# Optimization experiments

Hardware: AMD Instinct MI355X
Metric: run time of the kernel (lower is better)

The kernel has to match this reference:

```python
import jax, jax.numpy as jnp
import numpy as np

SEG = 24      # segment_size
NH = 8        # n_heads
THETA = 10000.0


def setup_inputs() -> dict:
    key = jax.random.key(0)
    ks = jax.random.split(key, 6)
    B, T, H, W, D = 8, 96, 32, 32, 64
    in_dim = SEG * D          # 1536
    hid_dim = (SEG // 2) * D  # 768
    n_seg = T // SEG          # 4
    x = jax.random.normal(ks[0], (B, T, H, W, D), dtype=jnp.float32)
    # rotary frequencies: freqs_cis[t, j] = exp(i * t * theta^{-2j/hid_dim})
    inv = 1.0 / (THETA ** (np.arange(0, hid_dim, 2, dtype=np.float32) / hid_dim))
    ang = np.arange(n_seg, dtype=np.float32)[:, None] * inv[None, :]  # (n, hid/2)
    freqs_cos = jnp.asarray(np.cos(ang), dtype=jnp.float32)
    freqs_sin = jnp.asarray(np.sin(ang), dtype=jnp.float32)
    s = 0.02
    Wq = jax.random.normal(ks[1], (in_dim, hid_dim), dtype=jnp.float32) * s
    Wk = jax.random.normal(ks[2], (in_dim, hid_dim), dtype=jnp.float32) * s
    Wv = jax.random.normal(ks[3], (in_dim, hid_dim), dtype=jnp.float32) * s
    Wo = jax.random.normal(ks[4], (hid_dim, in_dim), dtype=jnp.float32) * s
    bo = jnp.zeros((in_dim,), dtype=jnp.float32)
    return {"x": x, "freqs_cos": freqs_cos, "freqs_sin": freqs_sin,
            "Wq": Wq, "Wk": Wk, "Wv": Wv, "Wo": Wo, "bo": bo}


def _rope(q, cos, sin):
    # q: (b, n, hid); pairs (even, odd) rotated by complex multiply
    q2 = q.reshape(*q.shape[:-1], -1, 2)
    qr = q2[..., 0] * cos - q2[..., 1] * sin
    qi = q2[..., 0] * sin + q2[..., 1] * cos
    return jnp.stack([qr, qi], axis=-1).reshape(q.shape)


def reference(x, freqs_cos, freqs_sin, Wq, Wk, Wv, Wo, bo):
    B, T, H, W, D = x.shape
    n = T // SEG
    hid = Wq.shape[1]
    hd = hid // NH
    # (b t h w d) -> ((b h w) n (p d)) ; T divisible by SEG so no padding
    xr = jnp.transpose(x, (0, 2, 3, 1, 4)).reshape(B * H * W, T, D)
    xs = xr.reshape(B * H * W, n, SEG * D)
    q = jnp.einsum('bne,eh->bnh', xs, Wq)
    k = jnp.einsum('bne,eh->bnh', xs, Wk)
    v = jnp.einsum('bne,eh->bnh', xs, Wv)
    cos, sin = freqs_cos[:n][None], freqs_sin[:n][None]  # (1, n, hid/2)
    q = _rope(q, cos, sin)
    k = _rope(k, cos, sin)
    # split heads: b n (h d) -> b h n d
    def heads(t):
        return jnp.transpose(t.reshape(B * H * W, n, NH, hd), (0, 2, 1, 3))
    qh, kh, vh = heads(q), heads(k), heads(v)
    scores = jnp.einsum('bhnd,bhmd->bhnm', qh, kh) / jnp.sqrt(jnp.float32(hd))
    attn = jax.nn.softmax(scores, axis=-1)
    o = jnp.einsum('bhnm,bhmd->bhnd', attn, vh)
    o = jnp.transpose(o, (0, 2, 1, 3)).reshape(B * H * W, n, hid)
    o = jnp.einsum('bnh,he->bne', o, Wo) + bo
    # b n (p d) -> b (n p) d -> (B,T,H,W,D)
    o = o.reshape(B * H * W, T, D)
    o = o.reshape(B, H, W, T, D)
    return jnp.transpose(o, (0, 3, 1, 2, 4))
```

## Files before the change

### kernel.cpp

```cpp
#include <hip/hip_runtime.h>
#include <hip/hip_bf16.h>

using bf16 = __hip_bfloat16;
using short8 = __attribute__((ext_vector_type(8))) short;
using floatx4 = __attribute__((ext_vector_type(4))) float;

#define NSEG 4
#define HID 768
#define INDIM 1536
#define NQKV 2304
#define NHEADS 8
#define HD 96

__device__ inline unsigned short f2b(float v) {
  union { float f; unsigned u; } c; c.f = v;
  unsigned r = c.u + 0x7FFF + ((c.u >> 16) & 1);
  return (unsigned short)(r >> 16);
}

__device__ inline void gload16(const void* g, void* l) {
  __builtin_amdgcn_global_load_lds(
      (const __attribute__((address_space(1))) unsigned int*)g,
      (__attribute__((address_space(3))) unsigned int*)l, 16, 0, 0);
}

__global__ __launch_bounds__(256) void transpose_w(
    const float* __restrict__ src, bf16* __restrict__ dst, int K, int C) {
  __shared__ unsigned short tile[32][33];
  const int c0 = blockIdx.x * 32, k0 = blockIdx.y * 32;
  const int tx = threadIdx.x, ty = threadIdx.y;
#pragma unroll
  for (int i = 0; i < 4; ++i)
    tile[ty + 8 * i][tx] = f2b(src[(size_t)(k0 + ty + 8 * i) * C + c0 + tx]);
  __syncthreads();
  unsigned short* d = (unsigned short*)dst;
#pragma unroll
  for (int i = 0; i < 4; ++i)
    d[(size_t)(c0 + ty + 8 * i) * K + k0 + tx] = tile[tx][ty + 8 * i];
}

__global__ __launch_bounds__(256) void convert_x(
    const float* __restrict__ x, bf16* __restrict__ xb) {
  const size_t i = ((size_t)blockIdx.x * 256 + threadIdx.x) * 8;
  float4 a = *(const float4*)(x + i);
  float4 b = *(const float4*)(x + i + 4);
  union { uint4 u; unsigned short s[8]; } r;
  r.s[0] = f2b(a.x); r.s[1] = f2b(a.y); r.s[2] = f2b(a.z); r.s[3] = f2b(a.w);
  r.s[4] = f2b(b.x); r.s[5] = f2b(b.y); r.s[6] = f2b(b.z); r.s[7] = f2b(b.w);
  *(uint4*)(xb + i) = r.u;
}

__global__ __launch_bounds__(256, 2) void gemm_qkv(
    const bf16* __restrict__ xb, const bf16* __restrict__ wT,
    bf16* __restrict__ qkv) {
  __shared__ __align__(16) short As[128 * 32];
  __shared__ __align__(16) short Bs[128 * 32];
  const int tid = threadIdx.x;
  const int n0 = blockIdx.x * 128;
  const int m0 = blockIdx.y * 128;
  const int lane = tid & 63, wave = tid >> 6;
  const int wm = (wave >> 1) * 64, wn = (wave & 1) * 64;
  const int l15 = lane & 15, quad = lane >> 4;
  const int srow = wave * 16 + (lane >> 2);
  const int sch = (lane & 3) * 8;
  floatx4 acc[4][4] = {};

  const int mA0 = m0 + srow, mA1 = m0 + 64 + srow;
  const int rA0 = mA0 >> 2, nA0 = mA0 & 3;
  const int rA1 = mA1 >> 2, nA1 = mA1 & 3;
  const size_t baseA0 =
      ((size_t)((rA0 >> 10) * 96 + nA0 * 24) * 1024 + (rA0 & 1023)) * 64;
  const size_t baseA1 =
      ((size_t)((rA1 >> 10) * 96 + nA1 * 24) * 1024 + (rA1 & 1023)) * 64;
  const bf16* bB0 = wT + (size_t)(n0 + srow) * INDIM + sch;
  const bf16* bB1 = wT + (size_t)(n0 + 64 + srow) * INDIM + sch;

  short* asb0 = &As[wave * 512];
  short* asb1 = &As[2048 + wave * 512];
  short* bsb0 = &Bs[wave * 512];
  short* bsb1 = &Bs[2048 + wave * 512];

  for (int kt = 0; kt < 48; ++kt) {
    const int k0 = kt * 32;
    const int p = kt >> 1;
    const int dlo = (kt & 1) * 32 + sch;
    __syncthreads();
    gload16(xb + baseA0 + (size_t)p * 65536 + dlo, asb0);
    gload16(xb + baseA1 + (size_t)p * 65536 + dlo, asb1);
    gload16(bB0 + k0, bsb0);
    gload16(bB1 + k0, bsb1);
    __syncthreads();
    short8 af[4], bg[4];
#pragma unroll
    for (int t = 0; t < 4; ++t) {
      af[t] = *(const short8*)&As[(wm + t * 16 + l15) * 32 + quad * 8];
      bg[t] = *(const short8*)&Bs[(wn + t * 16 + l15) * 32 + quad * 8];
    }
#pragma unroll
    for (int ti = 0; ti < 4; ++ti)
#pragma unroll
      for (int tj = 0; tj < 4; ++tj)
        acc[ti][tj] = __builtin_amdgcn_mfma_f32_16x16x32_bf16(
            af[ti], bg[tj], acc[ti][tj], 0, 0, 0);
  }
#pragma unroll
  for (int ti = 0; ti < 4; ++ti)
#pragma unroll
    for (int tj = 0; tj < 4; ++tj)
#pragma unroll
      for (int reg = 0; reg < 4; ++reg) {
        const int row = m0 + wm + ti * 16 + quad * 4 + reg;
        const int col = n0 + wn + tj * 16 + l15;
        qkv[(size_t)row * NQKV + col] = __float2bfloat16(acc[ti][tj][reg]);
      }
}

__global__ __launch_bounds__(256) void attn_kernel(
    const bf16* __restrict__ qkv, const float* __restrict__ fcos,
    const float* __restrict__ fsin, bf16* __restrict__ obuf) {
  constexpr int SF_LD = 2312;
  __shared__ float sf[NSEG][SF_LD];
  __shared__ float ssc[NHEADS][NSEG][NSEG];
  __shared__ float sat[NHEADS][NSEG][NSEG];
  const int r = blockIdx.x;
  const int tid = threadIdx.x;
  const bf16* base = qkv + (size_t)r * NSEG * NQKV;

  for (int cid = tid; cid < (NSEG * NQKV) / 8; cid += 256) {
    const int n = cid / (NQKV / 8);
    const int c = (cid % (NQKV / 8)) * 8;
    uint4 u = *(const uint4*)(base + (size_t)n * NQKV + c);
    const bf16* h = reinterpret_cast<const bf16*>(&u);
#pragma unroll
    for (int j = 0; j < 8; ++j) sf[n][c + j] = __bfloat162float(h[j]);
  }
  __syncthreads();

  for (int idx = tid; idx < NSEG * (HID / 2); idx += 256) {
    const int n = idx / (HID / 2), j = idx % (HID / 2);
    const float c = fcos[n * (HID / 2) + j];
    const float s = fsin[n * (HID / 2) + j];
    float q0 = sf[n][2 * j], q1 = sf[n][2 * j + 1];
    sf[n][2 * j] = q0 * c - q1 * s;
    sf[n][2 * j + 1] = q0 * s + q1 * c;
    float k0 = sf[n][HID + 2 * j], k1 = sf[n][HID + 2 * j + 1];
    sf[n][HID + 2 * j] = k0 * c - k1 * s;
    sf[n][HID + 2 * j + 1] = k0 * s + k1 * c;
  }
  __syncthreads();

  if (tid < 128) {
    const int h = tid >> 4, n = (tid >> 2) & 3, m = tid & 3;
    const float* qp = &sf[n][h * HD];
    const float* kp = &sf[m][HID + h * HD];
    float s = 0.f;
#pragma unroll 8
    for (int i = 0; i < HD; ++i) s += qp[i] * kp[i];
    ssc[h][n][m] = s * 0.10206207261596575f;
  }
  __syncthreads();

  if (tid < 32) {
    const int h = tid >> 2, n = tid & 3;
    float mx = ssc[h][n][0];
#pragma unroll
    for (int m = 1; m < 4; ++m) mx = fmaxf(mx, ssc[h][n][m]);
    float e[4], sum = 0.f;
#pragma unroll
    for (int m = 0; m < 4; ++m) { e[m] = __expf(ssc[h][n][m] - mx); sum += e[m]; }
    const float inv = 1.f / sum;
#pragma unroll
    for (int m = 0; m < 4; ++m) sat[h][n][m] = e[m] * inv;
  }
  __syncthreads();

  for (int idx = tid; idx < NSEG * HID; idx += 256) {
    const int n = idx / HID, c = idx % HID, h = c / HD;
    float s = 0.f;
#pragma unroll
    for (int m = 0; m < 4; ++m) s += sat[h][n][m] * sf[m][2 * HID + c];
    obuf[((size_t)r * NSEG + n) * HID + c] = __float2bfloat16(s);
  }
}

__global__ __launch_bounds__(256, 2) void gemm_out(
    const bf16* __restrict__ A, const bf16* __restrict__ wT,
    const float* __restrict__ bo, float* __restrict__ out) {
  __shared__ __align__(16) short As[128 * 32];
  __shared__ __align__(16) short Bs[128 * 32];
  const int tid = threadIdx.x;
  const int n0 = blockIdx.x * 128;
  const int m0 = blockIdx.y * 128;
  const int lane = tid & 63, wave = tid >> 6;
  const int wm = (wave >> 1) * 64, wn = (wave & 1) * 64;
  const int l15 = lane & 15, quad = lane >> 4;
  const int srow = wave * 16 + (lane >> 2);
  const int sch = (lane & 3) * 8;
  floatx4 acc[4][4] = {};

  const bf16* aB0 = A + (size_t)(m0 + srow) * HID + sch;
  const bf16* aB1 = A + (size_t)(m0 + 64 + srow) * HID + sch;
  const bf16* bB0 = wT + (size_t)(n0 + srow) * HID + sch;
  const bf16* bB1 = wT + (size_t)(n0 + 64 + srow) * HID + sch;

  short* asb0 = &As[wave * 512];
  short* asb1 = &As[2048 + wave * 512];
  short* bsb0 = &Bs[wave * 512];
  short* bsb1 = &Bs[2048 + wave * 512];

  for (int kt = 0; kt < 24; ++kt) {
    const int k0 = kt * 32;
    __syncthreads();
    gload16(aB0 + k0, asb0);
    gload16(aB1 + k0, asb1);
    gload16(bB0 + k0, bsb0);
    gload16(bB1 + k0, bsb1);
    __syncthreads();
    short8 af[4], bg[4];
#pragma unroll
    for (int t = 0; t < 4; ++t) {
      af[t] = *(const short8*)&As[(wm + t * 16 + l15) * 32 + quad * 8];
      bg[t] = *(const short8*)&Bs[(wn + t * 16 + l15) * 32 + quad * 8];
    }
#pragma unroll
    for (int ti = 0; ti < 4; ++ti)
#pragma unroll
      for (int tj = 0; tj < 4; ++tj)
        acc[ti][tj] = __builtin_amdgcn_mfma_f32_16x16x32_bf16(
            af[ti], bg[tj], acc[ti][tj], 0, 0, 0);
  }
#pragma unroll
  for (int ti = 0; ti < 4; ++ti)
#pragma unroll
    for (int tj = 0; tj < 4; ++tj)
#pragma unroll
      for (int reg = 0; reg < 4; ++reg) {
        const int row = m0 + wm + ti * 16 + quad * 4 + reg;
        const int col = n0 + wn + tj * 16 + l15;
        const float v = acc[ti][tj][reg] + bo[col];
        const int r = row >> 2, n = row & 3;
        const int b = r >> 10, hw = r & 1023;
        const int p = col >> 6, d = col & 63;
        const size_t dst =
            ((size_t)((b * 96 + n * 24 + p) * 1024 + hw)) * 64 + d;
        out[dst] = v;
      }
}

extern "C" void kernel_launch(void* const* d_in, const int* in_sizes, int n_in,
                              void* d_out, int out_size, void* d_ws,
                              size_t ws_size, hipStream_t stream) {
  const float* x = (const float*)d_in[0];
  const float* fcos = (const float*)d_in[1];
  const float* fsin = (const float*)d_in[2];
  const float* Wq = (const float*)d_in[3];
  const float* Wk = (const float*)d_in[4];
  const float* Wv = (const float*)d_in[5];
  const float* Wo = (const float*)d_in[6];
  const float* bo = (const float*)d_in[7];
  float* out = (float*)d_out;

  char* ws = (char*)d_ws;
  bf16* wqkvT = (bf16*)ws;
  bf16* woT = (bf16*)(ws + 7077888);
  bf16* qkv = (bf16*)(ws + 9437184);
  bf16* obuf = (bf16*)(ws + 160432128);
  bf16* xb = (bf16*)d_out;

  dim3 tb(32, 8);
  transpose_w<<<dim3(24, 48), tb, 0, stream>>>(Wq, wqkvT, INDIM, HID);
  transpose_w<<<dim3(24, 48), tb, 0, stream>>>(Wk, wqkvT + (size_t)HID * INDIM, INDIM, HID);
  transpose_w<<<dim3(24, 48), tb, 0, stream>>>(Wv, wqkvT + (size_t)2 * HID * INDIM, INDIM, HID);
  transpose_w<<<dim3(48, 24), tb, 0, stream>>>(Wo, woT, HID, INDIM);

  convert_x<<<24576, 256, 0, stream>>>(x, xb);
  gemm_qkv<<<dim3(18, 256), 256, 0, stream>>>(xb, wqkvT, qkv);
  attn_kernel<<<8192, 256, 0, stream>>>(qkv, fcos, fsin, obuf);
  gemm_out<<<dim3(12, 256), 256, 0, stream>>>(obuf, woT, bo, out);
}
```

Measured before the change: 827.2 us.

## Rewrite QKV and output GEMMs with 256x256 tiles, double-buffered swizzled LDS pipeline

Both GEMMs move from 128x128 tiles with two syncthreads per 32-wide K step to 256x256 tiles on 512 threads. They use a 64-wide K step and double-buffered LDS filled by direct global-to-LDS loads, interleaved with MFMA phases under explicit vmcnt waits and barriers. LDS addresses are XOR-swizzled to avoid bank conflicts, blocks are remapped for L2 locality, and s_setprio is raised around the MFMA bursts. This aims to hide memory latency and raise arithmetic intensity, at the cost of 128KB LDS per block, high register pressure, and delicate manual synchronisation.

```diff
diff --git a/kernel.cpp b/kernel.cpp
--- a/kernel.cpp
+++ b/kernel.cpp
@@ -23,6 +23,43 @@
       (const __attribute__((address_space(1))) unsigned int*)g,
       (__attribute__((address_space(3))) unsigned int*)l, 16, 0, 0);
 }
+
+#define MEMFENCE asm volatile("" ::: "memory")
+#define BARRIER do { MEMFENCE; __builtin_amdgcn_s_barrier(); MEMFENCE; } while (0)
+
+#define PHASE(par, q, LOADB, STAGES, VMW) do {                                 \
+    short8 a00 = *(const short8*)(lA + (par)*65536 + (q)*2048);                \
+    short8 a01 = *(const short8*)(lA + (par)*65536 + (q)*2048 + 16384);        \
+    short8 a10 = *(const short8*)(lA + (par)*65536 + (q)*2048 + 1024);         \
+    short8 a11 = *(const short8*)(lA + (par)*65536 + (q)*2048 + 1024 + 16384); \
+    if (LOADB) {                                                               \
+      _Pragma("unroll")                                                        \
+      for (int fn = 0; fn < 4; ++fn) {                                         \
+        bfr[fn][0] = *(const short8*)(lB + (par)*65536 + fn*1024);             \
+        bfr[fn][1] = *(const short8*)(lB + (par)*65536 + fn*1024 + 16384);     \
+      }                                                                        \
+    }                                                                          \
+    STAGES;                                                                    \
+    BARRIER;                                                                   \
+    __builtin_amdgcn_s_setprio(1);                                             \
+    _Pragma("unroll")                                                          \
+    for (int fn = 0; fn < 4; ++fn) {                                           \
+      acc[2*(q)][fn]   = __builtin_amdgcn_mfma_f32_16x16x32_bf16(              \
+          a00, bfr[fn][0], acc[2*(q)][fn], 0, 0, 0);                           \
+      acc[2*(q)][fn]   = __builtin_amdgcn_mfma_f32_16x16x32_bf16(              \
+          a01, bfr[fn][1], acc[2*(q)][fn], 0, 0, 0);                           \
+      acc[2*(q)+1][fn] = __builtin_amdgcn_mfma_f32_16x16x32_bf16(              \
+          a10, bfr[fn][0], acc[2*(q)+1][fn], 0, 0, 0);                         \
+      acc[2*(q)+1][fn] = __builtin_amdgcn_mfma_f32_16x16x32_bf16(              \
+          a11, bfr[fn][1], acc[2*(q)+1][fn], 0, 0, 0);                         \
+    }                                                                          \
+    __builtin_amdgcn_s_setprio(0);                                             \
+    VMW;                                                                       \
+    BARRIER;                                                                   \
+  } while (0)
+
+#define VM4 do { asm volatile("s_waitcnt vmcnt(4)" ::: "memory"); } while (0)
+#define VM0 do { asm volatile("s_waitcnt vmcnt(0)" ::: "memory"); } while (0)
 
 __global__ __launch_bounds__(256) void transpose_w(
     const float* __restrict__ src, bf16* __restrict__ dst, int K, int C) {
@@ -50,68 +87,84 @@
   *(uint4*)(xb + i) = r.u;
 }
 
-__global__ __launch_bounds__(256, 2) void gemm_qkv(
+__global__ __launch_bounds__(512, 2) void gemm_qkv(
     const bf16* __restrict__ xb, const bf16* __restrict__ wT,
     bf16* __restrict__ qkv) {
-  __shared__ __align__(16) short As[128 * 32];
-  __shared__ __align__(16) short Bs[128 * 32];
+  __shared__ __align__(16) char lds[131072];
   const int tid = threadIdx.x;
-  const int n0 = blockIdx.x * 128;
-  const int m0 = blockIdx.y * 128;
   const int lane = tid & 63, wave = tid >> 6;
-  const int wm = (wave >> 1) * 64, wn = (wave & 1) * 64;
+  const int wr = wave >> 2, wc = wave & 3;
   const int l15 = lane & 15, quad = lane >> 4;
+
+  const int lt = (blockIdx.x & 7) * 144 + (blockIdx.x >> 3);
+  const int n0 = (lt % 9) * 256;
+  const int m0 = (lt / 9) * 256;
+
   const int srow = wave * 16 + (lane >> 2);
-  const int sch = (lane & 3) * 8;
-  floatx4 acc[4][4] = {};
-
-  const int mA0 = m0 + srow, mA1 = m0 + 64 + srow;
-  const int rA0 = mA0 >> 2, nA0 = mA0 & 3;
-  const int rA1 = mA1 >> 2, nA1 = mA1 & 3;
-  const size_t baseA0 =
-      ((size_t)((rA0 >> 10) * 96 + nA0 * 24) * 1024 + (rA0 & 1023)) * 64;
-  const size_t baseA1 =
-      ((size_t)((rA1 >> 10) * 96 + nA1 * 24) * 1024 + (rA1 & 1023)) * 64;
-  const bf16* bB0 = wT + (size_t)(n0 + srow) * INDIM + sch;
-  const bf16* bB1 = wT + (size_t)(n0 + 64 + srow) * INDIM + sch;
-
-  short* asb0 = &As[wave * 512];
-  short* asb1 = &As[2048 + wave * 512];
-  short* bsb0 = &Bs[wave * 512];
-  short* bsb1 = &Bs[2048 + wave * 512];
-
-  for (int kt = 0; kt < 48; ++kt) {
-    const int k0 = kt * 32;
-    const int p = kt >> 1;
-    const int dlo = (kt & 1) * 32 + sch;
-    __syncthreads();
-    gload16(xb + baseA0 + (size_t)p * 65536 + dlo, asb0);
-    gload16(xb + baseA1 + (size_t)p * 65536 + dlo, asb1);
-    gload16(bB0 + k0, bsb0);
-    gload16(bB1 + k0, bsb1);
-    __syncthreads();
-    short8 af[4], bg[4];
-#pragma unroll
-    for (int t = 0; t < 4; ++t) {
-      af[t] = *(const short8*)&As[(wm + t * 16 + l15) * 32 + quad * 8];
-      bg[t] = *(const short8*)&Bs[(wn + t * 16 + l15) * 32 + quad * 8];
-    }
-#pragma unroll
-    for (int ti = 0; ti < 4; ++ti)
-#pragma unroll
-      for (int tj = 0; tj < 4; ++tj)
-        acc[ti][tj] = __builtin_amdgcn_mfma_f32_16x16x32_bf16(
-            af[ti], bg[tj], acc[ti][tj], 0, 0, 0);
-  }
-#pragma unroll
-  for (int ti = 0; ti < 4; ++ti)
-#pragma unroll
-    for (int tj = 0; tj < 4; ++tj)
+  const int dswz = ((lane & 3) * 8) ^ ((lane & 32) >> 1);
+  const bf16* asrc[2];
+  const bf16* bsrc[2];
+#pragma unroll
+  for (int h = 0; h < 2; ++h) {
+    const int m = m0 + h * 128 + srow;
+    const int r = m >> 2, n = m & 3;
+    const int b = r >> 10, hw = r & 1023;
+    asrc[h] = xb + ((size_t)((b * 96 + n * 24) * 1024 + hw)) * 64 + dswz;
+    bsrc[h] = wT + (size_t)(n0 + h * 128 + srow) * INDIM + dswz;
+  }
+  char* sdst = lds + wave * 1024;
+
+#define STAGE_QA(kt, h) do {                                   \
+    char* d_ = sdst + (((kt) & 1) * 65536) + (h) * 8192;       \
+    const bf16* s_ = asrc[h] + (size_t)(kt) * 65536;           \
+    gload16(s_, d_);                                           \
+    gload16(s_ + 32, d_ + 16384);                              \
+  } while (0)
+#define STAGE_QB(kt, h) do {                                   \
+    char* d_ = sdst + 32768 + (((kt) & 1) * 65536) + (h) * 8192; \
+    const bf16* s_ = bsrc[h] + (size_t)(kt) * 64;              \
+    gload16(s_, d_);                                           \
+    gload16(s_ + 32, d_ + 16384);                              \
+  } while (0)
+
+  const int lofs = l15 * 64 + ((quad * 16) ^ ((l15 & 8) << 2));
+  const char* lA = lds + wr * 8192 + lofs;
+  const char* lB = lds + 32768 + wc * 4096 + lofs;
+
+  floatx4 acc[8][4] = {};
+  short8 bfr[4][2];
+
+  STAGE_QB(0, 0); STAGE_QB(0, 1); STAGE_QA(0, 0); STAGE_QA(0, 1);
+  STAGE_QB(1, 0); STAGE_QB(1, 1);
+  VM4;
+  BARRIER;
+
+  const int NKT = 24;
+  for (int i = 0; i < 12; ++i) {
+    const int a = 2 * i;
+    PHASE(0, 0, 1, { STAGE_QA(a + 1, 0); }, {});
+    PHASE(0, 1, 0, { STAGE_QA(a + 1, 1); }, {});
+    PHASE(0, 2, 0, { if (a + 2 < NKT) STAGE_QB(a + 2, 0); }, {});
+    PHASE(0, 3, 0, { if (a + 2 < NKT) STAGE_QB(a + 2, 1); },
+          { if (a + 2 < NKT) VM4; else VM0; });
+    PHASE(1, 0, 1, { if (a + 2 < NKT) STAGE_QA(a + 2, 0); }, {});
+    PHASE(1, 1, 0, { if (a + 2 < NKT) STAGE_QA(a + 2, 1); }, {});
+    PHASE(1, 2, 0, { if (a + 3 < NKT) STAGE_QB(a + 3, 0); }, {});
+    PHASE(1, 3, 0, { if (a + 3 < NKT) STAGE_QB(a + 3, 1); },
+          { if (a + 3 < NKT) VM4; else VM0; });
+  }
+#undef STAGE_QA
+#undef STAGE_QB
+
+#pragma unroll
+  for (int fm = 0; fm < 8; ++fm)
+#pragma unroll
+    for (int fn = 0; fn < 4; ++fn)
 #pragma unroll
       for (int reg = 0; reg < 4; ++reg) {
-        const int row = m0 + wm + ti * 16 + quad * 4 + reg;
-        const int col = n0 + wn + tj * 16 + l15;
-        qkv[(size_t)row * NQKV + col] = __float2bfloat16(acc[ti][tj][reg]);
+        const int row = m0 + wr * 128 + fm * 16 + quad * 4 + reg;
+        const int col = n0 + wc * 64 + fn * 16 + l15;
+        qkv[(size_t)row * NQKV + col] = __float2bfloat16(acc[fm][fn][reg]);
       }
 }
 
@@ -183,61 +236,81 @@
   }
 }
 
-__global__ __launch_bounds__(256, 2) void gemm_out(
-    const bf16* __restrict__ A, const bf16* __restrict__ wT,
+__global__ __launch_bounds__(512, 2) void gemm_out(
+    const bf16* __restrict__ Ao, const bf16* __restrict__ wT,
     const float* __restrict__ bo, float* __restrict__ out) {
-  __shared__ __align__(16) short As[128 * 32];
-  __shared__ __align__(16) short Bs[128 * 32];
+  __shared__ __align__(16) char lds[131072];
   const int tid = threadIdx.x;
-  const int n0 = blockIdx.x * 128;
-  const int m0 = blockIdx.y * 128;
   const int lane = tid & 63, wave = tid >> 6;
-  const int wm = (wave >> 1) * 64, wn = (wave & 1) * 64;
+  const int wr = wave >> 2, wc = wave & 3;
   const int l15 = lane & 15, quad = lane >> 4;
+
+  const int lt = (blockIdx.x & 7) * 96 + (blockIdx.x >> 3);
+  const int n0 = (lt % 6) * 256;
+  const int m0 = (lt / 6) * 256;
+
   const int srow = wave * 16 + (lane >> 2);
-  const int sch = (lane & 3) * 8;
-  floatx4 acc[4][4] = {};
-
-  const bf16* aB0 = A + (size_t)(m0 + srow) * HID + sch;
-  const bf16* aB1 = A + (size_t)(m0 + 64 + srow) * HID + sch;
-  const bf16* bB0 = wT + (size_t)(n0 + srow) * HID + sch;
-  const bf16* bB1 = wT + (size_t)(n0 + 64 + srow) * HID + sch;
-
-  short* asb0 = &As[wave * 512];
-  short* asb1 = &As[2048 + wave * 512];
-  short* bsb0 = &Bs[wave * 512];
-  short* bsb1 = &Bs[2048 + wave * 512];
-
-  for (int kt = 0; kt < 24; ++kt) {
-    const int k0 = kt * 32;
-    __syncthreads();
-    gload16(aB0 + k0, asb0);
-    gload16(aB1 + k0, asb1);
-    gload16(bB0 + k0, bsb0);
-    gload16(bB1 + k0, bsb1);
-    __syncthreads();
-    short8 af[4], bg[4];
-#pragma unroll
-    for (int t = 0; t < 4; ++t) {
-      af[t] = *(const short8*)&As[(wm + t * 16 + l15) * 32 + quad * 8];
-      bg[t] = *(const short8*)&Bs[(wn + t * 16 + l15) * 32 + quad * 8];
-    }
-#pragma unroll
-    for (int ti = 0; ti < 4; ++ti)
-#pragma unroll
-      for (int tj = 0; tj < 4; ++tj)
-        acc[ti][tj] = __builtin_amdgcn_mfma_f32_16x16x32_bf16(
-            af[ti], bg[tj], acc[ti][tj], 0, 0, 0);
-  }
-#pragma unroll
-  for (int ti = 0; ti < 4; ++ti)
-#pragma unroll
-    for (int tj = 0; tj < 4; ++tj)
+  const int dswz = ((lane & 3) * 8) ^ ((lane & 32) >> 1);
+  const bf16* asrc[2];
+  const bf16* bsrc[2];
+#pragma unroll
+  for (int h = 0; h < 2; ++h) {
+    asrc[h] = Ao + (size_t)(m0 + h * 128 + srow) * HID + dswz;
+    bsrc[h] = wT + (size_t)(n0 + h * 128 + srow) * HID + dswz;
+  }
+  char* sdst = lds + wave * 1024;
+
+#define STAGE_OA(kt, h) do {                                   \
+    char* d_ = sdst + (((kt) & 1) * 65536) + (h) * 8192;       \
+    const bf16* s_ = asrc[h] + (size_t)(kt) * 64;              \
+    gload16(s_, d_);                                           \
+    gload16(s_ + 32, d_ + 16384);                              \
+  } while (0)
+#define STAGE_OB(kt, h) do {                                   \
+    char* d_ = sdst + 32768 + (((kt) & 1) * 65536) + (h) * 8192; \
+    const bf16* s_ = bsrc[h] + (size_t)(kt) * 64;              \
+    gload16(s_, d_);                                           \
+    gload16(s_ + 32, d_ + 16384);                              \
+  } while (0)
+
+  const int lofs = l15 * 64 + ((quad * 16) ^ ((l15 & 8) << 2));
+  const char* lA = lds + wr * 8192 + lofs;
+  const char* lB = lds + 32768 + wc * 4096 + lofs;
+
+  floatx4 acc[8][4] = {};
+  short8 bfr[4][2];
+
+  STAGE_OB(0, 0); STAGE_OB(0, 1); STAGE_OA(0, 0); STAGE_OA(0, 1);
+  STAGE_OB(1, 0); STAGE_OB(1, 1);
+  VM4;
+  BARRIER;
+
+  const int NKT = 12;
+  for (int i = 0; i < 6; ++i) {
+    const int a = 2 * i;
+    PHASE(0, 0, 1, { STAGE_OA(a + 1, 0); }, {});
+    PHASE(0, 1, 0, { STAGE_OA(a + 1, 1); }, {});
+    PHASE(0, 2, 0, { if (a + 2 < NKT) STAGE_OB(a + 2, 0); }, {});
+    PHASE(0, 3, 0, { if (a + 2 < NKT) STAGE_OB(a + 2, 1); },
+          { if (a + 2 < NKT) VM4; else VM0; });
+    PHASE(1, 0, 1, { if (a + 2 < NKT) STAGE_OA(a + 2, 0); }, {});
+    PHASE(1, 1, 0, { if (a + 2 < NKT) STAGE_OA(a + 2, 1); }, {});
+    PHASE(1, 2, 0, { if (a + 3 < NKT) STAGE_OB(a + 3, 0); }, {});
+    PHASE(1, 3, 0, { if (a + 3 < NKT) STAGE_OB(a + 3, 1); },
+          { if (a + 3 < NKT) VM4; else VM0; });
+  }
+#undef STAGE_OA
+#undef STAGE_OB
+
+#pragma unroll
+  for (int fm = 0; fm < 8; ++fm)
+#pragma unroll
+    for (int fn = 0; fn < 4; ++fn)
 #pragma unroll
       for (int reg = 0; reg < 4; ++reg) {
-        const int row = m0 + wm + ti * 16 + quad * 4 + reg;
-        const int col = n0 + wn + tj * 16 + l15;
-        const float v = acc[ti][tj][reg] + bo[col];
+        const int row = m0 + wr * 128 + fm * 16 + quad * 4 + reg;
+        const int col = n0 + wc * 64 + fn * 16 + l15;
+        const float v = acc[fm][fn][reg] + bo[col];
         const int r = row >> 2, n = row & 3;
         const int b = r >> 10, hw = r & 1023;
         const int p = col >> 6, d = col & 63;
@@ -274,7 +347,7 @@
   transpose_w<<<dim3(48, 24), tb, 0, stream>>>(Wo, woT, HID, INDIM);
 
   convert_x<<<24576, 256, 0, stream>>>(x, xb);
-  gemm_qkv<<<dim3(18, 256), 256, 0, stream>>>(xb, wqkvT, qkv);
+  gemm_qkv<<<1152, 512, 0, stream>>>(xb, wqkvT, qkv);
   attn_kernel<<<8192, 256, 0, stream>>>(qkv, fcos, fsin, obuf);
-  gemm_out<<<dim3(12, 256), 256, 0, stream>>>(obuf, woT, bo, out);
-}
+  gemm_out<<<768, 512, 0, stream>>>(obuf, woT, bo, out);
+}
```

New measurement: 706.5 us. 1.17x faster.
